# Kernel tuning notes

Hardware: AMD Instinct MI355X
Metric: run time of the kernel (lower is better)

Reference implementation:

```python
import jax, jax.numpy as jnp
import numpy as np

B, H, W, L, C = 4, 64, 64, 64, 64
NB, BS, F = 8, 8, 1          # num_blocks, block_size, hidden_size_factor
R, ALPHA = 8, 1.0            # lora_r, lora_alpha
M, T = 32, 8                 # modes, temporal_modes
SCALE = 1.0 / (BS * BS * F)  # param init scale from the module


def setup_inputs() -> dict:
    key = jax.random.key(0)
    ks = jax.random.split(key, 14)
    d = {"x": jax.random.normal(ks[0], (B, H, W, L, C), jnp.float32)}
    d["w1"] = SCALE * jax.random.uniform(ks[1], (2, NB, BS, BS * F), jnp.float32)
    d["b1"] = SCALE * jax.random.uniform(ks[2], (2, NB, BS * F), jnp.float32)
    d["w2"] = SCALE * jax.random.uniform(ks[3], (2, NB, BS * F, BS), jnp.float32)
    d["b2"] = SCALE * jax.random.uniform(ks[4], (2, NB, BS), jnp.float32)
    names = ["la1rA", "la1rB", "la1iA", "la1iB", "la2rA", "la2rB", "la2iA", "la2iB"]
    shapes = [(NB, BS, R), (NB, R, BS * F), (NB, BS, R), (NB, R, BS * F),
              (NB, BS * F, R), (NB, R, BS), (NB, BS * F, R), (NB, R, BS)]
    for i, (n, s) in enumerate(zip(names, shapes)):
        d[n] = 0.02 * jax.random.normal(ks[5 + i], s, jnp.float32)
    return d


def _afno(x, w1, b1, w2, b2, la1rA, la1rB, la1iA, la1iB, la2rA, la2rB, la2iA, la2iB):
    s = ALPHA / R
    # effective per-block weights: base + LoRA low-rank update  [NB, in, out]
    W1r = w1[0] + s * jnp.einsum('nir,nro->nio', la1rA, la1rB)
    W1i = w1[1] + s * jnp.einsum('nir,nro->nio', la1iA, la1iB)
    W2r = w2[0] + s * jnp.einsum('nir,nro->nio', la2rA, la2rB)
    W2i = w2[1] + s * jnp.einsum('nir,nro->nio', la2iA, la2iB)

    xf = jnp.fft.rfftn(x, axes=(1, 2, 3), norm='ortho')      # [B,H,W,L//2+1,C] complex
    Lh = xf.shape[3]
    xs = xf[:, :M, :M, :T].reshape(B, M, M, T, NB, BS)        # truncated modes, block split
    xr, xi = xs.real, xs.imag

    def lin(v, Wb, bb):  # block-diagonal linear: [...,n,i] x [n,i,o] + [n,o]
        return jnp.einsum('bxyzni,nio->bxyzno', v, Wb) + bb

    gelu = lambda t: jax.nn.gelu(t, approximate=False)
    o1r = gelu(lin(xr, W1r, b1[0]) - lin(xi, W1i, b1[1]))
    o1i = gelu(lin(xi, W1r, b1[0]) + lin(xr, W1i, b1[1]))
    o2r = lin(o1r, W2r, b2[0]) - lin(o1i, W2i, b2[1])
    o2i = lin(o1i, W2r, b2[0]) + lin(o1r, W2i, b2[1])

    o2 = (o2r + 1j * o2i).reshape(B, M, M, T, C)
    full = jnp.zeros((B, H, W, Lh, C), dtype=xf.dtype).at[:, :M, :M, :T].set(o2)
    out = jnp.fft.irfftn(full, s=(H, W, L), axes=(1, 2, 3), norm='ortho')
    return out + x


def reference(x, w1, b1, w2, b2, la1rA, la1rB, la1iA, la1iB, la2rA, la2rB, la2iA, la2iB):
    return _afno(x, w1, b1, w2, b2, la1rA, la1rB, la1iA, la1iB, la2rA, la2rB, la2iA, la2iB)
```

## Files before the change

### kernel.cpp

```cpp
#include <hip/hip_runtime.h>
#include <math.h>


#define PI2_64 0.09817477042468103f

__device__ __forceinline__ float gelu_exact(float t) {
    return 0.5f * t * (1.0f + erff(t * 0.7071067811865475f));
}

__global__ void __launch_bounds__(256) k1a_dft_l(const float* __restrict__ x,
                                                 float* __restrict__ y1f) {
    __shared__ float2 twT[8][64];
    int tid = threadIdx.x;
    {
        int k = tid >> 6, l = tid & 63;
        float s, c;
        sincosf(PI2_64 * (float)((k * l) & 63), &s, &c);
        twT[k][l] = make_float2(c, s);
        int k2 = k + 4;
        sincosf(PI2_64 * (float)((k2 * l) & 63), &s, &c);
        twT[k2][l] = make_float2(c, s);
    }
    __syncthreads();

    int bid = blockIdx.x;
    int w8 = bid & 7, bh = bid >> 3;
    int cp = tid & 31, wl = tid >> 5;
    int w = w8 * 8 + wl;
    const float* xp = x + (size_t)(bh * 64 + w) * 4096 + 2 * cp;

    float4 A[8];
#pragma unroll
    for (int kl = 0; kl < 8; ++kl) A[kl] = make_float4(0.f, 0.f, 0.f, 0.f);

    for (int l0 = 0; l0 < 64; l0 += 4) {
        float2 v0 = *(const float2*)(xp + (l0 + 0) * 64);
        float2 v1 = *(const float2*)(xp + (l0 + 1) * 64);
        float2 v2 = *(const float2*)(xp + (l0 + 2) * 64);
        float2 v3 = *(const float2*)(xp + (l0 + 3) * 64);
#pragma unroll
        for (int kl = 0; kl < 8; ++kl) {
            float2 t0 = twT[kl][l0 + 0];
            float2 t1 = twT[kl][l0 + 1];
            float2 t2 = twT[kl][l0 + 2];
            float2 t3 = twT[kl][l0 + 3];
            A[kl].x += v0.x * t0.x;  A[kl].y -= v0.x * t0.y;
            A[kl].z += v0.y * t0.x;  A[kl].w -= v0.y * t0.y;
            A[kl].x += v1.x * t1.x;  A[kl].y -= v1.x * t1.y;
            A[kl].z += v1.y * t1.x;  A[kl].w -= v1.y * t1.y;
            A[kl].x += v2.x * t2.x;  A[kl].y -= v2.x * t2.y;
            A[kl].z += v2.y * t2.x;  A[kl].w -= v2.y * t2.y;
            A[kl].x += v3.x * t3.x;  A[kl].y -= v3.x * t3.y;
            A[kl].z += v3.y * t3.x;  A[kl].w -= v3.y * t3.y;
        }
    }
    float4* y1 = (float4*)y1f;
    size_t base = (size_t)bh * 16384 + (size_t)w * 32 + cp;
#pragma unroll
    for (int kl = 0; kl < 8; ++kl)
        y1[base + kl * 2048] = A[kl];
}

__global__ void __launch_bounds__(256) k1b_dft_w(const float* __restrict__ y1f,
                                                 float* __restrict__ y2f) {
    __shared__ float4 sD[64 * 32];
    __shared__ float2 twT[32][64];
    int tid = threadIdx.x;
#pragma unroll
    for (int e = 0; e < 8; ++e) {
        int idx = e * 256 + tid;
        int k = idx >> 6, l = idx & 63;
        float s, c;
        sincosf(PI2_64 * (float)((k * l) & 63), &s, &c);
        twT[k][l] = make_float2(c, s);
    }
    int pos = blockIdx.x;
    int kl = pos & 7, bh = pos >> 3;
    const float4* src = (const float4*)y1f + (size_t)pos * 2048;
#pragma unroll
    for (int r = 0; r < 8; ++r)
        sD[r * 256 + tid] = src[r * 256 + tid];
    __syncthreads();

    int cp = tid & 31, kwg = tid >> 5;
    float4 acc[4];
#pragma unroll
    for (int i = 0; i < 4; ++i) acc[i] = make_float4(0.f, 0.f, 0.f, 0.f);

    for (int w = 0; w < 64; ++w) {
        float4 d = sD[w * 32 + cp];
#pragma unroll
        for (int i = 0; i < 4; ++i) {
            float2 t = twT[kwg * 4 + i][w];
            acc[i].x += d.x * t.x + d.y * t.y;
            acc[i].y += d.y * t.x - d.x * t.y;
            acc[i].z += d.z * t.x + d.w * t.y;
            acc[i].w += d.w * t.x - d.z * t.y;
        }
    }
    int b = bh >> 6, h = bh & 63;
    float4* y2 = (float4*)y2f;
#pragma unroll
    for (int i = 0; i < 4; ++i) {
        int kw = kwg * 4 + i;
        y2[((size_t)((b * 8 + kl) * 32 + kw) * 64 + h) * 32 + cp] = acc[i];
    }
}

__global__ void __launch_bounds__(256) kc_h_mlp(
        const float* __restrict__ y2f, float* __restrict__ z2f,
        const float* __restrict__ w1, const float* __restrict__ b1,
        const float* __restrict__ w2, const float* __restrict__ b2,
        const float* __restrict__ la1rA, const float* __restrict__ la1rB,
        const float* __restrict__ la1iA, const float* __restrict__ la1iB,
        const float* __restrict__ la2rA, const float* __restrict__ la2rB,
        const float* __restrict__ la2iA, const float* __restrict__ la2iB) {
    __shared__ float2 sD[64][64];
    __shared__ float2 sT[64][34];
    __shared__ float2 sM[32][66];
    __shared__ float  sW[4][512];
    __shared__ float  sb1[128], sb2[128];
    int tid = threadIdx.x;
    int pos = blockIdx.x;
    int kl = pos & 7, kw = (pos >> 3) & 31, b = pos >> 8;

#pragma unroll
    for (int r = 0; r < 8; ++r) {
        int idx = r * 256 + tid;
        int h = idx >> 5, kh = idx & 31;
        float sn, cs;
        sincosf(PI2_64 * (float)((h * kh) & 63), &sn, &cs);
        sT[h][kh] = make_float2(cs, -sn);
    }
    const float2* src = (const float2*)y2f + (size_t)((b * 8 + kl) * 32 + kw) * 4096;
#pragma unroll
    for (int r = 0; r < 8; ++r) {
        int f = r * 512 + tid * 2;
        *(float4*)(&sD[f >> 6][f & 63]) = *(const float4*)(src + f);
    }
    {
        const float* As[4]   = {la1rA, la1iA, la2rA, la2iA};
        const float* Bs[4]   = {la1rB, la1iB, la2rB, la2iB};
        const float* base[4] = {w1, w1 + 512, w2, w2 + 512};
#pragma unroll
        for (int e = 0; e < 8; ++e) {
            int flat = tid + e * 256;
            int mat = flat >> 9;
            int rem = flat & 511;
            int n = rem >> 6, i = (rem >> 3) & 7, o = rem & 7;
            const float* A  = As[mat] + n * 64 + i * 8;
            const float* Bp = Bs[mat] + n * 64 + o;
            float s = 0.f;
#pragma unroll
            for (int r = 0; r < 8; ++r) s += A[r] * Bp[r * 8];
            sW[mat][(i * 8 + o) * 8 + n] = base[mat][n * 64 + i * 8 + o] + 0.125f * s;
        }
        if (tid < 128) sb1[tid] = b1[tid];
        else           sb2[tid - 128] = b2[tid - 128];
    }
    __syncthreads();

    {
        int kh0 = (tid >> 5) * 4;
        int c0  = (tid & 31) * 2;
        float mr[4][2], mi[4][2];
#pragma unroll
        for (int i = 0; i < 4; ++i)
#pragma unroll
            for (int j = 0; j < 2; ++j) { mr[i][j] = 0.f; mi[i][j] = 0.f; }
        for (int h = 0; h < 64; ++h) {
            const float4* tT = (const float4*)(&sT[h][kh0]);
            float4 u0 = tT[0], u1 = tT[1];
            float4 d0 = *(const float4*)(&sD[h][c0]);
            float Tr[4] = {u0.x, u0.z, u1.x, u1.z};
            float Ti[4] = {u0.y, u0.w, u1.y, u1.w};
            float Dr[2] = {d0.x, d0.z};
            float Di[2] = {d0.y, d0.w};
#pragma unroll
            for (int i = 0; i < 4; ++i)
#pragma unroll
                for (int j = 0; j < 2; ++j) {
                    mr[i][j] += Tr[i] * Dr[j] - Ti[i] * Di[j];
                    mi[i][j] += Tr[i] * Di[j] + Ti[i] * Dr[j];
                }
        }
        const float sc = 1.0f / 512.0f;
#pragma unroll
        for (int i = 0; i < 4; ++i)
#pragma unroll
            for (int j = 0; j < 2; ++j)
                sM[kh0 + i][c0 + j] = make_float2(mr[i][j] * sc, mi[i][j] * sc);
    }
    __syncthreads();

    float2* sM2 = (float2*)&sD[0][0];
    {
        int kh = tid >> 3, n = tid & 7;
        float xr[8], xi[8];
#pragma unroll
        for (int i = 0; i < 8; ++i) {
            float2 v = sM[kh][n * 8 + i];
            xr[i] = v.x; xi[i] = v.y;
        }
        float o1r[8], o1i[8];
#pragma unroll
        for (int o = 0; o < 8; ++o) {
            float br = sb1[n * 8 + o], bi = sb1[64 + n * 8 + o];
            float sr = br - bi, si = br + bi;
#pragma unroll
            for (int i = 0; i < 8; ++i) {
                float wr = sW[0][(i * 8 + o) * 8 + n];
                float wi = sW[1][(i * 8 + o) * 8 + n];
                sr += xr[i] * wr - xi[i] * wi;
                si += xi[i] * wr + xr[i] * wi;
            }
            o1r[o] = gelu_exact(sr);
            o1i[o] = gelu_exact(si);
        }
#pragma unroll
        for (int o = 0; o < 8; ++o) {
            float br = sb2[n * 8 + o], bi = sb2[64 + n * 8 + o];
            float sr = br - bi, si = br + bi;
#pragma unroll
            for (int i = 0; i < 8; ++i) {
                float wr = sW[2][(i * 8 + o) * 8 + n];
                float wi = sW[3][(i * 8 + o) * 8 + n];
                sr += o1r[i] * wr - o1i[i] * wi;
                si += o1i[i] * wr + o1r[i] * wi;
            }
            sM2[kh * 66 + n * 8 + o] = make_float2(sr, si);
        }
    }
    __syncthreads();

    {
        int h0 = (tid >> 4) * 4;
        int c0 = (tid & 15) * 4;
        float orr[4][4], oii[4][4];
#pragma unroll
        for (int i = 0; i < 4; ++i)
#pragma unroll
            for (int j = 0; j < 4; ++j) { orr[i][j] = 0.f; oii[i][j] = 0.f; }
        for (int kh = 0; kh < 32; ++kh) {
            float2 T0 = sT[h0 + 0][kh];
            float2 T1 = sT[h0 + 1][kh];
            float2 T2 = sT[h0 + 2][kh];
            float2 T3 = sT[h0 + 3][kh];
            float Tr[4] = {T0.x, T1.x, T2.x, T3.x};
            float Ti[4] = {T0.y, T1.y, T2.y, T3.y};
            const float4* tM = (const float4*)(sM2 + kh * 66 + c0);
            float4 m0 = tM[0], m1 = tM[1];
            float Mr[4] = {m0.x, m0.z, m1.x, m1.z};
            float Mi[4] = {m0.y, m0.w, m1.y, m1.w};
#pragma unroll
            for (int i = 0; i < 4; ++i)
#pragma unroll
                for (int j = 0; j < 4; ++j) {
                    orr[i][j] += Tr[i] * Mr[j] + Ti[i] * Mi[j];
                    oii[i][j] += Tr[i] * Mi[j] - Ti[i] * Mr[j];
                }
        }
        float2* dst = (float2*)z2f + (size_t)((b * 8 + kl) * 32 + kw) * 4096;
#pragma unroll
        for (int i = 0; i < 4; ++i) {
            float4* d4 = (float4*)(dst + (h0 + i) * 64 + c0);
            d4[0] = make_float4(orr[i][0], oii[i][0], orr[i][1], oii[i][1]);
            d4[1] = make_float4(orr[i][2], oii[i][2], orr[i][3], oii[i][3]);
        }
    }
}

__global__ void __launch_bounds__(512, 4) k3_wl(const float* __restrict__ x,
                                                const float* __restrict__ z2f,
                                                float* __restrict__ outp) {
    __shared__ float4 sZ[8 * 32 * 16];
    __shared__ float2 twA[8][64];
    int tid = threadIdx.x;
    int bid = blockIdx.x;
    int b = bid >> 7, h = (bid >> 1) & 63, ch = bid & 1;
    int c0 = ch * 32;

    {
        int k = tid >> 6, l = tid & 63;
        float s, c;
        sincosf(PI2_64 * (float)((k * l) & 63), &s, &c);
        twA[k][l] = make_float2(c, s);
    }
    const float4* z2 = (const float4*)z2f;
#pragma unroll
    for (int k = 0; k < 8; ++k) {
        int idx = k * 512 + tid;
        int klkw = idx >> 4, cp = idx & 15;
        sZ[idx] = z2[(size_t)((b * 256 + klkw) * 64 + h) * 32 + ch * 16 + cp];
    }
    __syncthreads();

    int cp = tid & 15, wlo = tid >> 4;

    float4 zE[8], zO[8];
#pragma unroll
    for (int kl = 0; kl < 8; ++kl) {
        zE[kl] = make_float4(0.f, 0.f, 0.f, 0.f);
        zO[kl] = make_float4(0.f, 0.f, 0.f, 0.f);
    }
    float2 u = make_float2(1.f, 0.f);
    float2 su;
    {
        float s, c;
        sincosf(PI2_64 * (float)wlo, &s, &c);
        su = make_float2(c, s);
    }
    for (int kw = 0; kw < 32; kw += 2) {
#pragma unroll
        for (int kl = 0; kl < 8; ++kl) {
            float4 d = sZ[(kl * 32 + kw) * 16 + cp];
            zE[kl].x += d.x * u.x - d.y * u.y;
            zE[kl].y += d.y * u.x + d.x * u.y;
            zE[kl].z += d.z * u.x - d.w * u.y;
            zE[kl].w += d.w * u.x + d.z * u.y;
        }
        {
            float nr = u.x * su.x - u.y * su.y;
            float ni = u.y * su.x + u.x * su.y;
            u = make_float2(nr, ni);
        }
#pragma unroll
        for (int kl = 0; kl < 8; ++kl) {
            float4 d = sZ[(kl * 32 + kw + 1) * 16 + cp];
            zO[kl].x += d.x * u.x - d.y * u.y;
            zO[kl].y += d.y * u.x + d.x * u.y;
            zO[kl].z += d.z * u.x - d.w * u.y;
            zO[kl].w += d.w * u.x + d.z * u.y;
        }
        {
            float nr = u.x * su.x - u.y * su.y;
            float ni = u.y * su.x + u.x * su.y;
            u = make_float2(nr, ni);
        }
    }
#pragma unroll
    for (int kl = 0; kl < 8; ++kl) {
        float4 e = zE[kl], o = zO[kl];
        zE[kl] = make_float4(e.x + o.x, e.y + o.y, e.z + o.z, e.w + o.w);
        zO[kl] = make_float4(e.x - o.x, e.y - o.y, e.z - o.z, e.w - o.w);
    }

    float zAr0 = zE[0].x, zAr1 = zE[0].z;
    float zBr0 = zO[0].x, zBr1 = zO[0].z;
#pragma unroll
    for (int kl = 1; kl < 8; ++kl) {
        zE[kl].x *= 2.f; zE[kl].y *= 2.f; zE[kl].z *= 2.f; zE[kl].w *= 2.f;
        zO[kl].x *= 2.f; zO[kl].y *= 2.f; zO[kl].z *= 2.f; zO[kl].w *= 2.f;
    }
    const size_t rowA = (size_t)((b * 64 + h) * 64 + wlo) * 4096;
    const size_t rowB = rowA + (size_t)32 * 4096;
    const float* xpA = x + rowA + c0 + 2 * cp;
    const float* xpB = x + rowB + c0 + 2 * cp;
    float* opA = outp + rowA + c0 + 2 * cp;
    float* opB = outp + rowB + c0 + 2 * cp;
    const float sc = 1.0f / 512.0f;

    float2 a0 = *(const float2*)(xpA + 0 * 64);
    float2 b0 = *(const float2*)(xpB + 0 * 64);
    float2 a1 = *(const float2*)(xpA + 1 * 64);
    float2 b1 = *(const float2*)(xpB + 1 * 64);
    for (int l = 0; l < 64; ++l) {
        int lp = (l + 2) & 63;
        float2 a2 = *(const float2*)(xpA + lp * 64);
        float2 b2 = *(const float2*)(xpB + lp * 64);
        float s0 = zAr0, s1 = zAr1, s2 = zBr0, s3 = zBr1;
#pragma unroll
        for (int kl = 1; kl < 8; ++kl) {
            float2 t = twA[kl][l];
            s0 += zE[kl].x * t.x - zE[kl].y * t.y;
            s1 += zE[kl].z * t.x - zE[kl].w * t.y;
            s2 += zO[kl].x * t.x - zO[kl].y * t.y;
            s3 += zO[kl].z * t.x - zO[kl].w * t.y;
        }
        *(float2*)(opA + l * 64) = make_float2(s0 * sc + a0.x, s1 * sc + a0.y);
        *(float2*)(opB + l * 64) = make_float2(s2 * sc + b0.x, s3 * sc + b0.y);
        a0 = a1; a1 = a2; b0 = b1; b1 = b2;
    }
}

extern "C" void kernel_launch(void* const* d_in, const int* in_sizes, int n_in,
                              void* d_out, int out_size, void* d_ws, size_t ws_size,
                              hipStream_t stream) {
    const float* x     = (const float*)d_in[0];
    const float* w1    = (const float*)d_in[1];
    const float* b1    = (const float*)d_in[2];
    const float* w2    = (const float*)d_in[3];
    const float* b2    = (const float*)d_in[4];
    const float* la1rA = (const float*)d_in[5];
    const float* la1rB = (const float*)d_in[6];
    const float* la1iA = (const float*)d_in[7];
    const float* la1iB = (const float*)d_in[8];
    const float* la2rA = (const float*)d_in[9];
    const float* la2rB = (const float*)d_in[10];
    const float* la2iA = (const float*)d_in[11];
    const float* la2iB = (const float*)d_in[12];
    float* out = (float*)d_out;

    float* ws = (float*)d_ws;
    float* y1 = ws;
    float* y2 = ws + 16777216;
    float* z2 = ws + 25165824;

    hipLaunchKernelGGL(k1a_dft_l, dim3(2048), dim3(256), 0, stream, x, y1);
    hipLaunchKernelGGL(k1b_dft_w, dim3(2048), dim3(256), 0, stream, y1, y2);
    hipLaunchKernelGGL(kc_h_mlp,  dim3(1024), dim3(256), 0, stream, y2, z2,
                       w1, b1, w2, b2, la1rA, la1rB, la1iA, la1iB,
                       la2rA, la2rB, la2iA, la2iB);
    hipLaunchKernelGGL(k3_wl,     dim3(512),  dim3(512), 0, stream, x, z2, out);
}
```

Before: 338.1 us.

## Apply radix-2 even/odd butterfly split to all truncated DFT stages

Uses the symmetry twiddle(k, n+32) = (-1)^k twiddle(k, n) to fold each 64-point truncated DFT into a 32-point sum over x[n]±x[n+32]. This applies to the L and W forward DFTs, the H forward and inverse DFTs inside the MLP kernel, and the final L inverse DFT. Twiddle tables shrink by half and multiply-add work in each stage roughly halves. The cost is extra butterfly adds, one more shared-memory pass with a barrier in the MLP kernel, and some register pressure from split accumulators.

```diff
diff --git a/kernel.cpp b/kernel.cpp
--- a/kernel.cpp
+++ b/kernel.cpp
@@ -10,16 +10,13 @@
 
 __global__ void __launch_bounds__(256) k1a_dft_l(const float* __restrict__ x,
                                                  float* __restrict__ y1f) {
-    __shared__ float2 twT[8][64];
+    __shared__ float2 twT[8][32];
     int tid = threadIdx.x;
-    {
-        int k = tid >> 6, l = tid & 63;
+    if (tid < 256) {
+        int k = tid >> 5, l = tid & 31;
         float s, c;
         sincosf(PI2_64 * (float)((k * l) & 63), &s, &c);
         twT[k][l] = make_float2(c, s);
-        int k2 = k + 4;
-        sincosf(PI2_64 * (float)((k2 * l) & 63), &s, &c);
-        twT[k2][l] = make_float2(c, s);
     }
     __syncthreads();
 
@@ -33,25 +30,25 @@
 #pragma unroll
     for (int kl = 0; kl < 8; ++kl) A[kl] = make_float4(0.f, 0.f, 0.f, 0.f);
 
-    for (int l0 = 0; l0 < 64; l0 += 4) {
-        float2 v0 = *(const float2*)(xp + (l0 + 0) * 64);
-        float2 v1 = *(const float2*)(xp + (l0 + 1) * 64);
-        float2 v2 = *(const float2*)(xp + (l0 + 2) * 64);
-        float2 v3 = *(const float2*)(xp + (l0 + 3) * 64);
+    for (int l0 = 0; l0 < 32; l0 += 2) {
+        float2 v0  = *(const float2*)(xp + (l0 + 0) * 64);
+        float2 v0p = *(const float2*)(xp + (l0 + 32) * 64);
+        float2 v1  = *(const float2*)(xp + (l0 + 1) * 64);
+        float2 v1p = *(const float2*)(xp + (l0 + 33) * 64);
+        float2 E0 = make_float2(v0.x + v0p.x, v0.y + v0p.y);
+        float2 O0 = make_float2(v0.x - v0p.x, v0.y - v0p.y);
+        float2 E1 = make_float2(v1.x + v1p.x, v1.y + v1p.y);
+        float2 O1 = make_float2(v1.x - v1p.x, v1.y - v1p.y);
 #pragma unroll
         for (int kl = 0; kl < 8; ++kl) {
-            float2 t0 = twT[kl][l0 + 0];
+            float2 t0 = twT[kl][l0];
             float2 t1 = twT[kl][l0 + 1];
-            float2 t2 = twT[kl][l0 + 2];
-            float2 t3 = twT[kl][l0 + 3];
-            A[kl].x += v0.x * t0.x;  A[kl].y -= v0.x * t0.y;
-            A[kl].z += v0.y * t0.x;  A[kl].w -= v0.y * t0.y;
-            A[kl].x += v1.x * t1.x;  A[kl].y -= v1.x * t1.y;
-            A[kl].z += v1.y * t1.x;  A[kl].w -= v1.y * t1.y;
-            A[kl].x += v2.x * t2.x;  A[kl].y -= v2.x * t2.y;
-            A[kl].z += v2.y * t2.x;  A[kl].w -= v2.y * t2.y;
-            A[kl].x += v3.x * t3.x;  A[kl].y -= v3.x * t3.y;
-            A[kl].z += v3.y * t3.x;  A[kl].w -= v3.y * t3.y;
+            float2 s0 = (kl & 1) ? O0 : E0;
+            float2 s1 = (kl & 1) ? O1 : E1;
+            A[kl].x += s0.x * t0.x;  A[kl].y -= s0.x * t0.y;
+            A[kl].z += s0.y * t0.x;  A[kl].w -= s0.y * t0.y;
+            A[kl].x += s1.x * t1.x;  A[kl].y -= s1.x * t1.y;
+            A[kl].z += s1.y * t1.x;  A[kl].w -= s1.y * t1.y;
         }
     }
     float4* y1 = (float4*)y1f;
@@ -64,12 +61,12 @@
 __global__ void __launch_bounds__(256) k1b_dft_w(const float* __restrict__ y1f,
                                                  float* __restrict__ y2f) {
     __shared__ float4 sD[64 * 32];
-    __shared__ float2 twT[32][64];
+    __shared__ float2 twT[32][32];
     int tid = threadIdx.x;
 #pragma unroll
-    for (int e = 0; e < 8; ++e) {
+    for (int e = 0; e < 4; ++e) {
         int idx = e * 256 + tid;
-        int k = idx >> 6, l = idx & 63;
+        int k = idx >> 5, l = idx & 31;
         float s, c;
         sincosf(PI2_64 * (float)((k * l) & 63), &s, &c);
         twT[k][l] = make_float2(c, s);
@@ -87,15 +84,19 @@
 #pragma unroll
     for (int i = 0; i < 4; ++i) acc[i] = make_float4(0.f, 0.f, 0.f, 0.f);
 
-    for (int w = 0; w < 64; ++w) {
-        float4 d = sD[w * 32 + cp];
+    for (int w = 0; w < 32; ++w) {
+        float4 d  = sD[w * 32 + cp];
+        float4 dp = sD[(w + 32) * 32 + cp];
+        float4 E = make_float4(d.x + dp.x, d.y + dp.y, d.z + dp.z, d.w + dp.w);
+        float4 O = make_float4(d.x - dp.x, d.y - dp.y, d.z - dp.z, d.w - dp.w);
 #pragma unroll
         for (int i = 0; i < 4; ++i) {
             float2 t = twT[kwg * 4 + i][w];
-            acc[i].x += d.x * t.x + d.y * t.y;
-            acc[i].y += d.y * t.x - d.x * t.y;
-            acc[i].z += d.z * t.x + d.w * t.y;
-            acc[i].w += d.w * t.x - d.z * t.y;
+            float4 s = (i & 1) ? O : E;
+            acc[i].x += s.x * t.x + s.y * t.y;
+            acc[i].y += s.y * t.x - s.x * t.y;
+            acc[i].z += s.z * t.x + s.w * t.y;
+            acc[i].w += s.w * t.x - s.z * t.y;
         }
     }
     int b = bh >> 6, h = bh & 63;
@@ -116,7 +117,7 @@
         const float* __restrict__ la2rA, const float* __restrict__ la2rB,
         const float* __restrict__ la2iA, const float* __restrict__ la2iB) {
     __shared__ float2 sD[64][64];
-    __shared__ float2 sT[64][34];
+    __shared__ float2 sT[32][34];
     __shared__ float2 sM[32][66];
     __shared__ float  sW[4][512];
     __shared__ float  sb1[128], sb2[128];
@@ -125,7 +126,7 @@
     int kl = pos & 7, kw = (pos >> 3) & 31, b = pos >> 8;
 
 #pragma unroll
-    for (int r = 0; r < 8; ++r) {
+    for (int r = 0; r < 4; ++r) {
         int idx = r * 256 + tid;
         int h = idx >> 5, kh = idx & 31;
         float sn, cs;
@@ -161,6 +162,20 @@
     __syncthreads();
 
     {
+        float4* sd4 = (float4*)&sD[0][0];
+#pragma unroll
+        for (int r = 0; r < 4; ++r) {
+            int idx = r * 256 + tid;
+            int h = idx >> 5, cq = idx & 31;
+            float4 a = sd4[h * 32 + cq];
+            float4 c = sd4[(h + 32) * 32 + cq];
+            sd4[h * 32 + cq]        = make_float4(a.x + c.x, a.y + c.y, a.z + c.z, a.w + c.w);
+            sd4[(h + 32) * 32 + cq] = make_float4(a.x - c.x, a.y - c.y, a.z - c.z, a.w - c.w);
+        }
+    }
+    __syncthreads();
+
+    {
         int kh0 = (tid >> 5) * 4;
         int c0  = (tid & 31) * 2;
         float mr[4][2], mi[4][2];
@@ -168,21 +183,25 @@
         for (int i = 0; i < 4; ++i)
 #pragma unroll
             for (int j = 0; j < 2; ++j) { mr[i][j] = 0.f; mi[i][j] = 0.f; }
-        for (int h = 0; h < 64; ++h) {
+        for (int h = 0; h < 32; ++h) {
+            float4 dE = *(const float4*)(&sD[h][c0]);
+            float4 dO = *(const float4*)(&sD[h + 32][c0]);
+            float Er[2] = {dE.x, dE.z}, Ei[2] = {dE.y, dE.w};
+            float Or[2] = {dO.x, dO.z}, Oi[2] = {dO.y, dO.w};
             const float4* tT = (const float4*)(&sT[h][kh0]);
             float4 u0 = tT[0], u1 = tT[1];
-            float4 d0 = *(const float4*)(&sD[h][c0]);
             float Tr[4] = {u0.x, u0.z, u1.x, u1.z};
             float Ti[4] = {u0.y, u0.w, u1.y, u1.w};
-            float Dr[2] = {d0.x, d0.z};
-            float Di[2] = {d0.y, d0.w};
-#pragma unroll
-            for (int i = 0; i < 4; ++i)
+#pragma unroll
+            for (int i = 0; i < 4; ++i) {
+                const float* Dr = (i & 1) ? Or : Er;
+                const float* Di = (i & 1) ? Oi : Ei;
 #pragma unroll
                 for (int j = 0; j < 2; ++j) {
                     mr[i][j] += Tr[i] * Dr[j] - Ti[i] * Di[j];
                     mi[i][j] += Tr[i] * Di[j] + Ti[i] * Dr[j];
                 }
+            }
         }
         const float sc = 1.0f / 512.0f;
 #pragma unroll
@@ -234,38 +253,52 @@
     __syncthreads();
 
     {
-        int h0 = (tid >> 4) * 4;
+        int h0 = (tid >> 4) * 2;
         int c0 = (tid & 15) * 4;
-        float orr[4][4], oii[4][4];
-#pragma unroll
-        for (int i = 0; i < 4; ++i)
-#pragma unroll
-            for (int j = 0; j < 4; ++j) { orr[i][j] = 0.f; oii[i][j] = 0.f; }
-        for (int kh = 0; kh < 32; ++kh) {
-            float2 T0 = sT[h0 + 0][kh];
-            float2 T1 = sT[h0 + 1][kh];
-            float2 T2 = sT[h0 + 2][kh];
-            float2 T3 = sT[h0 + 3][kh];
-            float Tr[4] = {T0.x, T1.x, T2.x, T3.x};
-            float Ti[4] = {T0.y, T1.y, T2.y, T3.y};
-            const float4* tM = (const float4*)(sM2 + kh * 66 + c0);
-            float4 m0 = tM[0], m1 = tM[1];
-            float Mr[4] = {m0.x, m0.z, m1.x, m1.z};
-            float Mi[4] = {m0.y, m0.w, m1.y, m1.w};
-#pragma unroll
-            for (int i = 0; i < 4; ++i)
-#pragma unroll
-                for (int j = 0; j < 4; ++j) {
-                    orr[i][j] += Tr[i] * Mr[j] + Ti[i] * Mi[j];
-                    oii[i][j] += Tr[i] * Mi[j] - Ti[i] * Mr[j];
-                }
+        float SEr[2][4], SEi[2][4], SOr[2][4], SOi[2][4];
+#pragma unroll
+        for (int r = 0; r < 2; ++r)
+#pragma unroll
+            for (int j = 0; j < 4; ++j) {
+                SEr[r][j] = 0.f; SEi[r][j] = 0.f;
+                SOr[r][j] = 0.f; SOi[r][j] = 0.f;
+            }
+        for (int khp = 0; khp < 16; ++khp) {
+#pragma unroll
+            for (int par = 0; par < 2; ++par) {
+                int kh = 2 * khp + par;
+                float2 T0 = sT[h0 + 0][kh];
+                float2 T1 = sT[h0 + 1][kh];
+                const float4* tM = (const float4*)(sM2 + kh * 66 + c0);
+                float4 m0 = tM[0], m1 = tM[1];
+                float Mr[4] = {m0.x, m0.z, m1.x, m1.z};
+                float Mi[4] = {m0.y, m0.w, m1.y, m1.w};
+                float (*Sr)[4] = par ? SOr : SEr;
+                float (*Si)[4] = par ? SOi : SEi;
+                float Tr[2] = {T0.x, T1.x};
+                float Ti[2] = {T0.y, T1.y};
+#pragma unroll
+                for (int r = 0; r < 2; ++r)
+#pragma unroll
+                    for (int j = 0; j < 4; ++j) {
+                        Sr[r][j] += Tr[r] * Mr[j] + Ti[r] * Mi[j];
+                        Si[r][j] += Tr[r] * Mi[j] - Ti[r] * Mr[j];
+                    }
+            }
         }
         float2* dst = (float2*)z2f + (size_t)((b * 8 + kl) * 32 + kw) * 4096;
 #pragma unroll
-        for (int i = 0; i < 4; ++i) {
-            float4* d4 = (float4*)(dst + (h0 + i) * 64 + c0);
-            d4[0] = make_float4(orr[i][0], oii[i][0], orr[i][1], oii[i][1]);
-            d4[1] = make_float4(orr[i][2], oii[i][2], orr[i][3], oii[i][3]);
+        for (int r = 0; r < 2; ++r) {
+            float4* dA = (float4*)(dst + (h0 + r) * 64 + c0);
+            dA[0] = make_float4(SEr[r][0] + SOr[r][0], SEi[r][0] + SOi[r][0],
+                                SEr[r][1] + SOr[r][1], SEi[r][1] + SOi[r][1]);
+            dA[1] = make_float4(SEr[r][2] + SOr[r][2], SEi[r][2] + SOi[r][2],
+                                SEr[r][3] + SOr[r][3], SEi[r][3] + SOi[r][3]);
+            float4* dB = (float4*)(dst + (h0 + 32 + r) * 64 + c0);
+            dB[0] = make_float4(SEr[r][0] - SOr[r][0], SEi[r][0] - SOi[r][0],
+                                SEr[r][1] - SOr[r][1], SEi[r][1] - SOi[r][1]);
+            dB[1] = make_float4(SEr[r][2] - SOr[r][2], SEi[r][2] - SOi[r][2],
+                                SEr[r][3] - SOr[r][3], SEi[r][3] - SOi[r][3]);
         }
     }
 }
@@ -274,14 +307,14 @@
                                                 const float* __restrict__ z2f,
                                                 float* __restrict__ outp) {
     __shared__ float4 sZ[8 * 32 * 16];
-    __shared__ float2 twA[8][64];
+    __shared__ float2 twA[8][32];
     int tid = threadIdx.x;
     int bid = blockIdx.x;
     int b = bid >> 7, h = (bid >> 1) & 63, ch = bid & 1;
     int c0 = ch * 32;
 
-    {
-        int k = tid >> 6, l = tid & 63;
+    if (tid < 256) {
+        int k = tid >> 5, l = tid & 31;
         float s, c;
         sincosf(PI2_64 * (float)((k * l) & 63), &s, &c);
         twA[k][l] = make_float2(c, s);
@@ -297,11 +330,11 @@
 
     int cp = tid & 15, wlo = tid >> 4;
 
-    float4 zE[8], zO[8];
+    float4 zA[8], zB[8];
 #pragma unroll
     for (int kl = 0; kl < 8; ++kl) {
-        zE[kl] = make_float4(0.f, 0.f, 0.f, 0.f);
-        zO[kl] = make_float4(0.f, 0.f, 0.f, 0.f);
+        zA[kl] = make_float4(0.f, 0.f, 0.f, 0.f);
+        zB[kl] = make_float4(0.f, 0.f, 0.f, 0.f);
     }
     float2 u = make_float2(1.f, 0.f);
     float2 su;
@@ -314,10 +347,10 @@
 #pragma unroll
         for (int kl = 0; kl < 8; ++kl) {
             float4 d = sZ[(kl * 32 + kw) * 16 + cp];
-            zE[kl].x += d.x * u.x - d.y * u.y;
-            zE[kl].y += d.y * u.x + d.x * u.y;
-            zE[kl].z += d.z * u.x - d.w * u.y;
-            zE[kl].w += d.w * u.x + d.z * u.y;
+            zA[kl].x += d.x * u.x - d.y * u.y;
+            zA[kl].y += d.y * u.x + d.x * u.y;
+            zA[kl].z += d.z * u.x - d.w * u.y;
+            zA[kl].w += d.w * u.x + d.z * u.y;
         }
         {
             float nr = u.x * su.x - u.y * su.y;
@@ -327,10 +360,10 @@
 #pragma unroll
         for (int kl = 0; kl < 8; ++kl) {
             float4 d = sZ[(kl * 32 + kw + 1) * 16 + cp];
-            zO[kl].x += d.x * u.x - d.y * u.y;
-            zO[kl].y += d.y * u.x + d.x * u.y;
-            zO[kl].z += d.z * u.x - d.w * u.y;
-            zO[kl].w += d.w * u.x + d.z * u.y;
+            zB[kl].x += d.x * u.x - d.y * u.y;
+            zB[kl].y += d.y * u.x + d.x * u.y;
+            zB[kl].z += d.z * u.x - d.w * u.y;
+            zB[kl].w += d.w * u.x + d.z * u.y;
         }
         {
             float nr = u.x * su.x - u.y * su.y;
@@ -340,17 +373,17 @@
     }
 #pragma unroll
     for (int kl = 0; kl < 8; ++kl) {
-        float4 e = zE[kl], o = zO[kl];
-        zE[kl] = make_float4(e.x + o.x, e.y + o.y, e.z + o.z, e.w + o.w);
-        zO[kl] = make_float4(e.x - o.x, e.y - o.y, e.z - o.z, e.w - o.w);
-    }
-
-    float zAr0 = zE[0].x, zAr1 = zE[0].z;
-    float zBr0 = zO[0].x, zBr1 = zO[0].z;
+        float4 e = zA[kl], o = zB[kl];
+        zA[kl] = make_float4(e.x + o.x, e.y + o.y, e.z + o.z, e.w + o.w);
+        zB[kl] = make_float4(e.x - o.x, e.y - o.y, e.z - o.z, e.w - o.w);
+    }
+
+    float zAr0 = zA[0].x, zAr1 = zA[0].z;
+    float zBr0 = zB[0].x, zBr1 = zB[0].z;
 #pragma unroll
     for (int kl = 1; kl < 8; ++kl) {
-        zE[kl].x *= 2.f; zE[kl].y *= 2.f; zE[kl].z *= 2.f; zE[kl].w *= 2.f;
-        zO[kl].x *= 2.f; zO[kl].y *= 2.f; zO[kl].z *= 2.f; zO[kl].w *= 2.f;
+        zA[kl].x *= 2.f; zA[kl].y *= 2.f; zA[kl].z *= 2.f; zA[kl].w *= 2.f;
+        zB[kl].x *= 2.f; zB[kl].y *= 2.f; zB[kl].z *= 2.f; zB[kl].w *= 2.f;
     }
     const size_t rowA = (size_t)((b * 64 + h) * 64 + wlo) * 4096;
     const size_t rowB = rowA + (size_t)32 * 4096;
@@ -360,26 +393,39 @@
     float* opB = outp + rowB + c0 + 2 * cp;
     const float sc = 1.0f / 512.0f;
 
-    float2 a0 = *(const float2*)(xpA + 0 * 64);
-    float2 b0 = *(const float2*)(xpB + 0 * 64);
-    float2 a1 = *(const float2*)(xpA + 1 * 64);
-    float2 b1 = *(const float2*)(xpB + 1 * 64);
-    for (int l = 0; l < 64; ++l) {
-        int lp = (l + 2) & 63;
-        float2 a2 = *(const float2*)(xpA + lp * 64);
-        float2 b2 = *(const float2*)(xpB + lp * 64);
-        float s0 = zAr0, s1 = zAr1, s2 = zBr0, s3 = zBr1;
-#pragma unroll
-        for (int kl = 1; kl < 8; ++kl) {
+    for (int l = 0; l < 32; ++l) {
+        float2 a0 = *(const float2*)(xpA + l * 64);
+        float2 a1 = *(const float2*)(xpA + (l + 32) * 64);
+        float2 b0 = *(const float2*)(xpB + l * 64);
+        float2 b1 = *(const float2*)(xpB + (l + 32) * 64);
+        float eA0 = 0.f, eA1 = 0.f, oA0 = 0.f, oA1 = 0.f;
+        float eB0 = 0.f, eB1 = 0.f, oB0 = 0.f, oB1 = 0.f;
+#pragma unroll
+        for (int kl = 2; kl < 8; kl += 2) {
             float2 t = twA[kl][l];
-            s0 += zE[kl].x * t.x - zE[kl].y * t.y;
-            s1 += zE[kl].z * t.x - zE[kl].w * t.y;
-            s2 += zO[kl].x * t.x - zO[kl].y * t.y;
-            s3 += zO[kl].z * t.x - zO[kl].w * t.y;
-        }
-        *(float2*)(opA + l * 64) = make_float2(s0 * sc + a0.x, s1 * sc + a0.y);
-        *(float2*)(opB + l * 64) = make_float2(s2 * sc + b0.x, s3 * sc + b0.y);
-        a0 = a1; a1 = a2; b0 = b1; b1 = b2;
+            eA0 += zA[kl].x * t.x - zA[kl].y * t.y;
+            eA1 += zA[kl].z * t.x - zA[kl].w * t.y;
+            eB0 += zB[kl].x * t.x - zB[kl].y * t.y;
+            eB1 += zB[kl].z * t.x - zB[kl].w * t.y;
+        }
+#pragma unroll
+        for (int kl = 1; kl < 8; kl += 2) {
+            float2 t = twA[kl][l];
+            oA0 += zA[kl].x * t.x - zA[kl].y * t.y;
+            oA1 += zA[kl].z * t.x - zA[kl].w * t.y;
+            oB0 += zB[kl].x * t.x - zB[kl].y * t.y;
+            oB1 += zB[kl].z * t.x - zB[kl].w * t.y;
+        }
+        float baseA0 = zAr0 + eA0, baseA1 = zAr1 + eA1;
+        float baseB0 = zBr0 + eB0, baseB1 = zBr1 + eB1;
+        *(float2*)(opA + l * 64) =
+            make_float2((baseA0 + oA0) * sc + a0.x, (baseA1 + oA1) * sc + a0.y);
+        *(float2*)(opA + (l + 32) * 64) =
+            make_float2((baseA0 - oA0) * sc + a1.x, (baseA1 - oA1) * sc + a1.y);
+        *(float2*)(opB + l * 64) =
+            make_float2((baseB0 + oB0) * sc + b0.x, (baseB1 + oB1) * sc + b0.y);
+        *(float2*)(opB + (l + 32) * 64) =
+            make_float2((baseB0 - oB0) * sc + b1.x, (baseB1 - oB1) * sc + b1.y);
     }
 }
 
```

Result: slower. 413.1 us (+22.2%).
